# Kernel tuning notes

Measured on AMD Instinct MI355X. Metric: run time of the kernel, lower is better.

The kernel has to match this reference:

```python
import jax, jax.numpy as jnp
import numpy as np

N = 131072       # total nodes (B graphs x P nodes)
P = 4096         # nodes per graph
B = 32           # graphs in batch
E = 2097152      # edges (avg degree 16)
IN_DIM = 64
HID = 128
OUT = 16
EPS = 1e-5
SLOPE = 0.01


def _degrees(idx):
    # structural degree, clamped to min 1 (as DGL GraphConv does)
    d = jax.ops.segment_sum(jnp.ones((E,), jnp.float32), idx, num_segments=N)
    return jnp.maximum(d, 1.0)


def _graph_conv(x, W, src, dst, ew):
    # DGL GraphConv, norm='both', bias=False, with scalar edge weights:
    # h = D_out^{-1/2} x ; m_v = sum_{(u->v)} w_e h_u ; out = (D_in^{-1/2} m) W
    h = x * jax.lax.rsqrt(_degrees(src))[:, None]
    m = jax.ops.segment_sum(ew[:, None] * h[src], dst, num_segments=N)  # [N, F]
    return (m * jax.lax.rsqrt(_degrees(dst))[:, None]) @ W


def _graph_norm(x, gamma, beta, alpha):
    # GraphNorm (Cai et al. / PyG, batch=None): stats over all nodes per feature
    mu = jnp.mean(x, axis=0)
    c = x - alpha * mu
    var = jnp.mean(c * c, axis=0)
    return c * jax.lax.rsqrt(var + EPS) * gamma + beta


def _mean_nodes(h, gid):
    # per-graph mean readout; every graph has exactly P nodes
    return jax.ops.segment_sum(h, gid, num_segments=B) / P


def setup_inputs() -> dict:
    key = jax.random.key(0)
    ks = jax.random.split(key, 8)
    src = jax.random.randint(ks[0], (E,), 0, N, dtype=jnp.int32)
    # keep edges within each 4096-node graph block (batched DGL graph)
    dst = (src // P) * P + jax.random.randint(ks[1], (E,), 0, P, dtype=jnp.int32)
    features = jax.random.normal(ks[2], (N, IN_DIM), jnp.float32)
    edge_weights = jax.random.uniform(ks[3], (E,), jnp.float32)
    # kaiming/xavier-scale init approximations
    W1 = jax.random.normal(ks[4], (IN_DIM, HID), jnp.float32) * np.sqrt(2.0 / IN_DIM)
    W2 = jax.random.normal(ks[5], (HID, HID), jnp.float32) * np.sqrt(2.0 / HID)
    Wc = jax.random.normal(ks[6], (OUT, 2 * HID), jnp.float32) * np.sqrt(1.0 / (2 * HID))
    ones = jnp.ones((HID,), jnp.float32)
    zeros = jnp.zeros((HID,), jnp.float32)
    return {
        'features': features, 'edge_weights': edge_weights, 'src': src, 'dst': dst,
        'W1': W1, 'W2': W2, 'Wc': Wc,
        'gamma1': ones, 'beta1': zeros, 'alpha1': ones,
        'gamma2': ones, 'beta2': zeros, 'alpha2': ones,
    }


def reference(features, edge_weights, src, dst, W1, W2, Wc,
              gamma1, beta1, alpha1, gamma2, beta2, alpha2):
    gid = jnp.arange(N, dtype=jnp.int32) // P  # node -> graph id
    h1 = _graph_conv(features, W1, src, dst, edge_weights)
    h1 = jax.nn.leaky_relu(_graph_norm(h1, gamma1, beta1, alpha1), SLOPE)
    r1 = _mean_nodes(h1, gid)                  # [B, HID]
    h2 = _graph_conv(h1, W2, src, dst, edge_weights)
    h2 = jax.nn.leaky_relu(_graph_norm(h2, gamma2, beta2, alpha2), SLOPE)
    r2 = _mean_nodes(h2, gid)                  # [B, HID]
    readouts = jnp.concatenate([r1, r2], axis=1)  # [B, 2*HID]
    return readouts @ Wc.T                     # [B, OUT]
```

## Files before the change

kernel.cpp:

```cpp
#include <hip/hip_runtime.h>
#include <hip/hip_fp16.h>

constexpr int NN   = 131072;
constexpr int PP   = 4096;
constexpr int BG   = 32;
constexpr int EE   = 2097152;
constexpr int IND  = 64;
constexpr int HH   = 128;
constexpr int CAP  = 81920;
constexpr float EPSV   = 1e-5f;
constexpr float SLOPEV = 0.01f;

typedef _Float16 h16x8 __attribute__((ext_vector_type(8)));
typedef float f32x4  __attribute__((ext_vector_type(4)));
typedef unsigned u32x4 __attribute__((ext_vector_type(4)));

__device__ __forceinline__ __half2 bits2h(unsigned u) { __half2 h; *(unsigned*)&h = u; return h; }
__device__ __forceinline__ unsigned h2bits(__half2 h) { return *(unsigned*)&h; }

template <int K>
__device__ __forceinline__ void packw_body(const float* __restrict__ W,
                                           unsigned short* __restrict__ pw, int t) {
    if (t >= K * 16) return;
    int lane = t & 63, nt = (t >> 6) & 7, kt = t >> 9;
    int kbase = kt * 32 + ((lane >> 4) & 3) * 8;
    int col   = nt * 16 + (lane & 15);
    for (int j = 0; j < 8; j++)
        pw[t * 8 + j] = __half_as_ushort(__float2half_rn(W[(kbase + j) * HH + col]));
}

__global__ __launch_bounds__(256) void k_prep(const float* __restrict__ features,
                                              unsigned* __restrict__ f16x,
                                              const float* __restrict__ W1,
                                              unsigned short* __restrict__ pw1,
                                              const float* __restrict__ W2,
                                              unsigned short* __restrict__ pw2,
                                              int* __restrict__ gcur,
                                              float* __restrict__ racc,
                                              unsigned* __restrict__ csr2) {
    int b = blockIdx.x, t = threadIdx.x;
    if (b < 8192) {
        int i = b * 256 + t;
        float4 v = ((const float4*)features)[i];
        __half2 lo = __floats2half2_rn(v.x, v.y);
        __half2 hi = __floats2half2_rn(v.z, v.w);
        ((uint2*)f16x)[i] = make_uint2(h2bits(lo), h2bits(hi));
        return;
    }
    if (b == 8192) {
        if (t < BG) gcur[t * 16] = t * CAP;
        for (int i = t; i < 2 * BG * HH; i += 256) racc[i] = 0.f;
        return;
    }
    if (b < 8197) { packw_body<64>(W1, pw1, (b - 8193) * 256 + t); return; }
    if (b < 8205) { packw_body<128>(W2, pw2, (b - 8197) * 256 + t); return; }
    ((uint4*)csr2)[(b - 8205) * 256 + t] = make_uint4(0, 0, 0, 0);
}

__global__ __launch_bounds__(256) void k_part(const int* __restrict__ src,
                                              const int* __restrict__ dst,
                                              const float* __restrict__ ew,
                                              int* __restrict__ gcur,
                                              uint2* __restrict__ recs) {
    __shared__ int cnt[32];
    __shared__ int start[32];
    __shared__ int gbase[32];
    __shared__ uint2 stage[4096];
    int t = threadIdx.x;
    int ebase = blockIdx.x * 4096;
    if (t < 32) cnt[t] = 0;
    __syncthreads();
    int es[16]; int ed[16]; float ev[16];
#pragma unroll
    for (int k = 0; k < 16; k++) {
        int e = ebase + k * 256 + t;
        es[k] = src[e]; ed[k] = dst[e]; ev[k] = ew[e];
        atomicAdd(&cnt[es[k] >> 12], 1);
    }
    __syncthreads();
    if (t == 0) {
        int run = 0;
        for (int g = 0; g < 32; g++) { start[g] = run; run += cnt[g]; }
    }
    __syncthreads();
    if (t < 32) {
        gbase[t] = atomicAdd(&gcur[t * 16], cnt[t]);
        cnt[t] = start[t];
    }
    __syncthreads();
#pragma unroll
    for (int k = 0; k < 16; k++) {
        int g = es[k] >> 12;
        int pos = atomicAdd(&cnt[g], 1);
        stage[pos] = make_uint2((unsigned)(es[k] & 4095) | ((unsigned)(ed[k] & 4095) << 12) |
                                ((unsigned)g << 24), __float_as_uint(ev[k]));
    }
    __syncthreads();
    for (int i = t; i < 4096; i += 256) {
        uint2 r = stage[i];
        int g = r.x >> 24;
        recs[gbase[g] + (i - start[g])] = r;
    }
}

__global__ __launch_bounds__(1024) void k_hist(const uint2* __restrict__ recs,
                                               const int* __restrict__ gcur,
                                               int* __restrict__ shist,
                                               int* __restrict__ dhist) {
    __shared__ int hs[4096];
    __shared__ int hd[4096];
    int t = threadIdx.x;
    int g = blockIdx.x >> 3, c = blockIdx.x & 7;
    int n = gcur[g * 16] - g * CAP;
    int lo = (n * c) >> 3, hi = (n * (c + 1)) >> 3;
    ((int4*)hs)[t] = make_int4(0, 0, 0, 0);
    ((int4*)hd)[t] = make_int4(0, 0, 0, 0);
    __syncthreads();
    const uint2* base = recs + (size_t)g * CAP;
    for (int i = lo + t; i < hi; i += 1024) {
        unsigned x = base[i].x;
        atomicAdd(&hs[x & 4095], 1);
        atomicAdd(&hd[(x >> 12) & 4095], 1);
    }
    __syncthreads();
    ((int4*)(shist + (size_t)blockIdx.x * 4096))[t] = ((int4*)hs)[t];
    ((int4*)(dhist + (size_t)blockIdx.x * 4096))[t] = ((int4*)hd)[t];
}

__global__ __launch_bounds__(1024) void k_offs(int* __restrict__ shist,
                                               int* __restrict__ dhist,
                                               float* __restrict__ rs_s,
                                               float* __restrict__ rsd,
                                               int* __restrict__ degd,
                                               int* __restrict__ offs) {
    __shared__ int partial[1024];
    int t = threadIdx.x, g = blockIdx.x;
    int sdeg[4] = {0, 0, 0, 0}, ddeg[4] = {0, 0, 0, 0};
#pragma unroll
    for (int c = 0; c < 8; c++) {
        int4 sv = ((const int4*)(shist + (size_t)(g * 8 + c) * 4096))[t];
        int4 dv = ((const int4*)(dhist + (size_t)(g * 8 + c) * 4096))[t];
        sdeg[0] += sv.x; sdeg[1] += sv.y; sdeg[2] += sv.z; sdeg[3] += sv.w;
        ddeg[0] += dv.x; ddeg[1] += dv.y; ddeg[2] += dv.z; ddeg[3] += dv.w;
    }
    int pdeg[4];
#pragma unroll
    for (int j = 0; j < 4; j++) {
        int idx = t * 4 + j;
        int vs = sdeg[j]; if (vs < 1) vs = 1;
        rs_s[g * PP + idx] = rsqrtf((float)vs);
        int vd = ddeg[j]; if (vd < 1) vd = 1;
        rsd[g * PP + idx]  = rsqrtf((float)vd);
        pdeg[j] = (ddeg[j] + 3) & ~3;
        degd[g * PP + idx] = pdeg[j];
    }
    partial[t] = pdeg[0] + pdeg[1] + pdeg[2] + pdeg[3];
    __syncthreads();
    for (int off = 1; off < 1024; off <<= 1) {
        int v = partial[t];
        int add = (t >= off) ? partial[t - off] : 0;
        __syncthreads();
        partial[t] = v + add;
        __syncthreads();
    }
    int run = (t == 0) ? 0 : partial[t - 1];
#pragma unroll
    for (int j = 0; j < 4; j++) {
        int idx = t * 4 + j;
        offs[g * PP + idx] = g * CAP + run;
        int nb = run;
        for (int c = 0; c < 8; c++) {
            size_t hidx = (size_t)(g * 8 + c) * 4096 + idx;
            int v = dhist[hidx];
            dhist[hidx] = nb;
            nb += v;
        }
        run += pdeg[j];
    }
}

__global__ __launch_bounds__(1024) void k_place(const uint2* __restrict__ recs,
                                                const int* __restrict__ gcur,
                                                const int* __restrict__ dhist,
                                                const float* __restrict__ rs_s,
                                                unsigned* __restrict__ csr2) {
    __shared__ int cur[4096];
    __shared__ float rss[4096];
    int t = threadIdx.x;
    int g = blockIdx.x >> 3, c = blockIdx.x & 7;
    int n = gcur[g * 16] - g * CAP;
    int lo = (n * c) >> 3, hi = (n * (c + 1)) >> 3;
    ((int4*)cur)[t] = ((const int4*)(dhist + (size_t)blockIdx.x * 4096))[t];
    ((float4*)rss)[t] = ((const float4*)(rs_s + (size_t)g * PP))[t];
    __syncthreads();
    const uint2* base = recs + (size_t)g * CAP;
    unsigned* cbase = csr2 + (size_t)g * CAP;
    for (int i = lo + t; i < hi; i += 1024) {
        uint2 r = base[i];
        int sl = r.x & 4095, dl = (r.x >> 12) & 4095;
        int pos = atomicAdd(&cur[dl], 1);
        float wf = __uint_as_float(r.y) * rss[sl];
        cbase[pos] = (unsigned)sl | ((unsigned)__half_as_ushort(__float2half(wf)) << 16);
    }
}

__device__ __forceinline__ void edge_acc(unsigned rec, uint2 q, __half2& P01, __half2& P23) {
    unsigned wb = __builtin_amdgcn_perm(rec, rec, 0x03020302u);
    __half2 w2 = bits2h(wb);
    P01 = __hfma2(w2, bits2h(q.x), P01);
    P23 = __hfma2(w2, bits2h(q.y), P23);
}

template <int ROWW>
__device__ __forceinline__ void gath(const uint2* __restrict__ gb, unsigned loff, u32x4 r,
                                     uint2& d0, uint2& d1, uint2& d2, uint2& d3) {
    d0 = gb[(r[0] & 4095u) * ROWW + loff];
    d1 = gb[(r[1] & 4095u) * ROWW + loff];
    d2 = gb[(r[2] & 4095u) * ROWW + loff];
    d3 = gb[(r[3] & 4095u) * ROWW + loff];
}

__device__ __forceinline__ void macc(u32x4 r, uint2 q0, uint2 q1, uint2 q2, uint2 q3,
                                     __half2& P01, __half2& P23) {
    edge_acc(r[0], q0, P01, P23); edge_acc(r[1], q1, P01, P23);
    edge_acc(r[2], q2, P01, P23); edge_acc(r[3], q3, P01, P23);
}

template <int ROWW>
__device__ __forceinline__ void agg_dual(const uint2* __restrict__ gb, unsigned loff,
                                         const u32x4* __restrict__ cs4,
                                         int oa, int ca, int ob, int cb,
                                         __half2& A01, __half2& A23,
                                         __half2& B01, __half2& B23) {
    A01 = __float2half2_rn(0.f); A23 = A01; B01 = A01; B23 = A01;
    unsigned a4 = ((unsigned)oa) >> 2, b4 = ((unsigned)ob) >> 2;
    int c0 = ca < cb ? ca : cb;
    int cm = ca < cb ? cb : ca;
    int nq = c0 >> 2;
    if (nq > 0) {
        u32x4 ra0 = __builtin_nontemporal_load(cs4 + a4);
        u32x4 rb0 = __builtin_nontemporal_load(cs4 + b4);
        u32x4 ra1 = __builtin_nontemporal_load(cs4 + a4 + 1);
        u32x4 rb1 = __builtin_nontemporal_load(cs4 + b4 + 1);
        uint2 A0, A1, A2, A3, B0, B1, B2, B3;
        uint2 C0, C1, C2, C3, D0, D1, D2, D3;
        gath<ROWW>(gb, loff, ra0, A0, A1, A2, A3);
        gath<ROWW>(gb, loff, rb0, B0, B1, B2, B3);
        int k = 0;
        for (; k + 2 <= nq; k += 2) {
            gath<ROWW>(gb, loff, ra1, C0, C1, C2, C3);
            gath<ROWW>(gb, loff, rb1, D0, D1, D2, D3);
            u32x4 ra2 = __builtin_nontemporal_load(cs4 + a4 + k + 2);
            u32x4 rb2 = __builtin_nontemporal_load(cs4 + b4 + k + 2);
            macc(ra0, A0, A1, A2, A3, A01, A23);
            macc(rb0, B0, B1, B2, B3, B01, B23);
            gath<ROWW>(gb, loff, ra2, A0, A1, A2, A3);
            gath<ROWW>(gb, loff, rb2, B0, B1, B2, B3);
            u32x4 ra3 = __builtin_nontemporal_load(cs4 + a4 + k + 3);
            u32x4 rb3 = __builtin_nontemporal_load(cs4 + b4 + k + 3);
            macc(ra1, C0, C1, C2, C3, A01, A23);
            macc(rb1, D0, D1, D2, D3, B01, B23);
            ra0 = ra2; rb0 = rb2; ra1 = ra3; rb1 = rb3;
        }
        if (k < nq) {
            macc(ra0, A0, A1, A2, A3, A01, A23);
            macc(rb0, B0, B1, B2, B3, B01, B23);
        }
    }
    if (cm > c0) {
        bool an = ca > cb;
        unsigned t4 = an ? a4 : b4;
        int kq1 = cm >> 2;
        __half2 E01 = __float2half2_rn(0.f), E23 = E01;
        int nq0 = c0 >> 2;
        u32x4 rr = __builtin_nontemporal_load(cs4 + t4 + nq0);
        for (int k = nq0; k < kq1; k++) {
            uint2 q0, q1, q2, q3;
            gath<ROWW>(gb, loff, rr, q0, q1, q2, q3);
            u32x4 nr = __builtin_nontemporal_load(cs4 + t4 + k + 1);
            macc(rr, q0, q1, q2, q3, E01, E23);
            rr = nr;
        }
        if (an) { A01 = __hadd2(A01, E01); A23 = __hadd2(A23, E23); }
        else    { B01 = __hadd2(B01, E01); B23 = __hadd2(B23, E23); }
    }
}

__global__ __launch_bounds__(256) void k_aggemm1(const unsigned* __restrict__ fx,
                                                 const unsigned* __restrict__ csr2,
                                                 const int* __restrict__ offs,
                                                 const int* __restrict__ degd,
                                                 const float* __restrict__ rsd,
                                                 const unsigned short* __restrict__ PW,
                                                 unsigned short* __restrict__ C,
                                                 float* __restrict__ part) {
    constexpr int WP = 36;
    __shared__ __align__(16) unsigned lds[64 * WP];
    __shared__ float s1[HH], s2[HH];
    int t = threadIdx.x;
    if (t < HH) { s1[t] = 0.f; s2[t] = 0.f; }
    int bid = blockIdx.x;
    int xcd = bid & 7, idx = bid >> 3;
    int g = xcd * 4 + (idx >> 6);
    int node0 = g * PP + (idx & 63) * 64;
    int lane = t & 63, wv = t >> 6;
    int q = lane >> 4, ql = lane & 15;
    const uint2* gb = (const uint2*)fx + (size_t)((unsigned)(g * PP)) * 16;
    const u32x4* cs4 = (const u32x4*)csr2;
#pragma unroll
    for (int p = 0; p < 2; p++) {
        int lrA = wv * 16 + p * 8 + q * 2;
        int va = node0 + lrA;
        int2 oo = *(const int2*)(offs + va);
        int2 dd = *(const int2*)(degd + va);
        __half2 A01, A23, B01, B23;
        agg_dual<16>(gb, (unsigned)ql, cs4, oo.x, dd.x, oo.y, dd.y, A01, A23, B01, B23);
        float2 rr2 = *(const float2*)(rsd + va);
        __half2 ha = __float2half2_rn(rr2.x), hb = __float2half2_rn(rr2.y);
        __half2 a0 = __hmul2(A01, ha), a1 = __hmul2(A23, ha);
        __half2 b0 = __hmul2(B01, hb), b1 = __hmul2(B23, hb);
        *(uint2*)&lds[lrA * WP + ql * 2]       = make_uint2(h2bits(a0), h2bits(a1));
        *(uint2*)&lds[(lrA + 1) * WP + ql * 2] = make_uint2(h2bits(b0), h2bits(b1));
    }
    __syncthreads();
    int m = lane & 15, quad = lane >> 4;
    h16x8 a[2];
#pragma unroll
    for (int kt = 0; kt < 2; kt++)
        a[kt] = *(const h16x8*)&lds[(wv * 16 + m) * WP + kt * 16 + quad * 4];
#pragma unroll
    for (int nt = 0; nt < 8; nt++) {
        f32x4 acc = {0.f, 0.f, 0.f, 0.f};
#pragma unroll
        for (int kt = 0; kt < 2; kt++) {
            h16x8 b = *(const h16x8*)(PW + ((size_t)(kt * 8 + nt) * 64 + lane) * 8);
            acc = __builtin_amdgcn_mfma_f32_16x16x32_f16(a[kt], b, acc, 0, 0, 0);
        }
        int col = nt * 16 + m;
        int r0 = node0 + wv * 16 + quad * 4;
        float ps = 0.f, pq = 0.f;
#pragma unroll
        for (int r = 0; r < 4; r++) {
            __builtin_nontemporal_store(
                (unsigned short)__half_as_ushort(__float2half_rn(acc[r])),
                &C[(size_t)(r0 + r) * HH + col]);
            ps += acc[r]; pq += acc[r] * acc[r];
        }
        atomicAdd(&s1[col], ps);
        atomicAdd(&s2[col], pq);
    }
    __syncthreads();
    if (t < HH) {
        __builtin_nontemporal_store(s1[t], &part[bid * 256 + t]);
        __builtin_nontemporal_store(s2[t], &part[bid * 256 + HH + t]);
    }
}

__global__ __launch_bounds__(256) void k_aggemm2(const unsigned* __restrict__ hsrc,
                                                 const unsigned* __restrict__ csr2,
                                                 const int* __restrict__ offs,
                                                 const int* __restrict__ degd,
                                                 const float* __restrict__ rsd,
                                                 const unsigned short* __restrict__ PW,
                                                 unsigned short* __restrict__ C,
                                                 float* __restrict__ part) {
    constexpr int WP = 68;
    __shared__ __align__(16) unsigned lds[64 * WP];
    __shared__ float s1[HH], s2[HH];
    int t = threadIdx.x;
    if (t < HH) { s1[t] = 0.f; s2[t] = 0.f; }
    int bid = blockIdx.x;
    int xcd = bid & 7, idx = bid >> 3;
    int g = xcd * 4 + (idx >> 6);
    int node0 = g * PP + (idx & 63) * 64;
    int lane = t & 63, wv = t >> 6;
    int half = lane >> 5, sl = lane & 31;
    const uint2* gb = (const uint2*)hsrc + (size_t)((unsigned)(g * PP)) * 32;
    const u32x4* cs4 = (const u32x4*)csr2;
#pragma unroll
    for (int p = 0; p < 4; p++) {
        int lrA = wv * 16 + p * 4 + half * 2;
        int va = node0 + lrA;
        int2 oo = *(const int2*)(offs + va);
        int2 dd = *(const int2*)(degd + va);
        __half2 A01, A23, B01, B23;
        agg_dual<32>(gb, (unsigned)sl, cs4, oo.x, dd.x, oo.y, dd.y, A01, A23, B01, B23);
        float2 rr2 = *(const float2*)(rsd + va);
        __half2 ha = __float2half2_rn(rr2.x), hb = __float2half2_rn(rr2.y);
        __half2 a0 = __hmul2(A01, ha), a1 = __hmul2(A23, ha);
        __half2 b0 = __hmul2(B01, hb), b1 = __hmul2(B23, hb);
        *(uint2*)&lds[lrA * WP + sl * 2]       = make_uint2(h2bits(a0), h2bits(a1));
        *(uint2*)&lds[(lrA + 1) * WP + sl * 2] = make_uint2(h2bits(b0), h2bits(b1));
    }
    __syncthreads();
    int m = lane & 15, quad = lane >> 4;
    h16x8 a[4];
#pragma unroll
    for (int kt = 0; kt < 4; kt++)
        a[kt] = *(const h16x8*)&lds[(wv * 16 + m) * WP + kt * 16 + quad * 4];
#pragma unroll
    for (int nt = 0; nt < 8; nt++) {
        f32x4 acc = {0.f, 0.f, 0.f, 0.f};
#pragma unroll
        for (int kt = 0; kt < 4; kt++) {
            h16x8 b = *(const h16x8*)(PW + ((size_t)(kt * 8 + nt) * 64 + lane) * 8);
            acc = __builtin_amdgcn_mfma_f32_16x16x32_f16(a[kt], b, acc, 0, 0, 0);
        }
        int col = nt * 16 + m;
        int r0 = node0 + wv * 16 + quad * 4;
        float ps = 0.f, pq = 0.f;
#pragma unroll
        for (int r = 0; r < 4; r++) {
            __builtin_nontemporal_store(
                (unsigned short)__half_as_ushort(__float2half_rn(acc[r])),
                &C[(size_t)(r0 + r) * HH + col]);
            ps += acc[r]; pq += acc[r] * acc[r];
        }
        atomicAdd(&s1[col], ps);
        atomicAdd(&s2[col], pq);
    }
    __syncthreads();
    if (t < HH) {
        __builtin_nontemporal_store(s1[t], &part[bid * 256 + t]);
        __builtin_nontemporal_store(s2[t], &part[bid * 256 + HH + t]);
    }
}

__global__ __launch_bounds__(256) void k_red(const float* __restrict__ part,
                                             float* __restrict__ pb) {
    int t = threadIdx.x, b = blockIdx.x;
    float s = 0.f;
    for (int r = 0; r < 32; r++) s += part[(size_t)(b * 32 + r) * 256 + t];
    pb[b * 256 + t] = s;
}

__global__ void k_coef(const float* __restrict__ pb, const float* __restrict__ gamma,
                       const float* __restrict__ beta, const float* __restrict__ alpha,
                       float* __restrict__ ab) {
    int t = threadIdx.x;
    float s = 0.f;
    for (int b = 0; b < 64; b++) s += pb[b * 256 + t];
    __shared__ float sh[256];
    sh[t] = s;
    __syncthreads();
    if (t < 128) {
        float mu = sh[t] * (1.f / NN);
        float e2 = sh[128 + t] * (1.f / NN);
        float al = alpha[t];
        float var = e2 - (2.f * al - al * al) * mu * mu;
        float a = rsqrtf(var + EPSV) * gamma[t];
        ab[t] = a;
        ab[HH + t] = beta[t] - al * mu * a;
    }
}

template <bool WRITE>
__global__ __launch_bounds__(256) void k_normro(const unsigned* __restrict__ h,
                                                const float* __restrict__ ab,
                                                float* __restrict__ racc,
                                                unsigned* __restrict__ f16o) {
    int fp = threadIdx.x & 63;
    int q  = threadIdx.x >> 6;
    int node0 = blockIdx.x * 64;
    int g = node0 / PP;
    float a0 = ab[2 * fp], a1 = ab[2 * fp + 1];
    float b0 = ab[HH + 2 * fp], b1 = ab[HH + 2 * fp + 1];
    float s0 = 0.f, s1 = 0.f;
    for (int i = q; i < 64; i += 4) {
        size_t idx = (size_t)(node0 + i) * 64 + fp;
        unsigned v = __builtin_nontemporal_load(&h[idx]);
        __half2 hv = bits2h(v);
        float x0 = fmaf(a0, __low2float(hv),  b0); x0 = x0 > 0.f ? x0 : SLOPEV * x0;
        float x1 = fmaf(a1, __high2float(hv), b1); x1 = x1 > 0.f ? x1 : SLOPEV * x1;
        if (WRITE) {
            __half2 o = __floats2half2_rn(x0, x1);
            __builtin_nontemporal_store(h2bits(o), &f16o[idx]);
        }
        s0 += x0; s1 += x1;
    }
    __shared__ float sh[512];
    sh[threadIdx.x] = s0;
    sh[256 + threadIdx.x] = s1;
    __syncthreads();
    if (q == 0) {
        float t0 = s0 + sh[64 + fp] + sh[128 + fp] + sh[192 + fp];
        float t1 = s1 + sh[256 + 64 + fp] + sh[256 + 128 + fp] + sh[256 + 192 + fp];
        atomicAdd(&racc[g * HH + 2 * fp],     t0);
        atomicAdd(&racc[g * HH + 2 * fp + 1], t1);
    }
}

__global__ void k_final(const float* __restrict__ racc1, const float* __restrict__ racc2,
                        const float* __restrict__ Wc, float* __restrict__ out) {
    int t = threadIdx.x;
    int b = t >> 4, o = t & 15;
    float acc = 0.f;
    for (int f = 0; f < HH; f++) acc += racc1[b * HH + f] * Wc[o * (2 * HH) + f];
    for (int f = 0; f < HH; f++) acc += racc2[b * HH + f] * Wc[o * (2 * HH) + HH + f];
    out[t] = acc * (1.f / PP);
}

extern "C" void kernel_launch(void* const* d_in, const int* in_sizes, int n_in,
                              void* d_out, int out_size, void* d_ws, size_t ws_size,
                              hipStream_t stream) {
    const float* features = (const float*)d_in[0];
    const float* ew       = (const float*)d_in[1];
    const int*   src      = (const int*)d_in[2];
    const int*   dst      = (const int*)d_in[3];
    const float* W1       = (const float*)d_in[4];
    const float* W2       = (const float*)d_in[5];
    const float* Wc       = (const float*)d_in[6];
    const float* gamma1   = (const float*)d_in[7];
    const float* beta1    = (const float*)d_in[8];
    const float* alpha1   = (const float*)d_in[9];
    const float* gamma2   = (const float*)d_in[10];
    const float* beta2    = (const float*)d_in[11];
    const float* alpha2   = (const float*)d_in[12];
    float* out = (float*)d_out;

    char* w = (char*)d_ws;
    int*    gcur   = (int*)(w + 0);
    float*  racc1  = (float*)(w + (16u << 10));
    float*  racc2  = (float*)(w + (32u << 10));
    float*  ab1    = (float*)(w + (48u << 10));
    float*  ab2    = (float*)(w + (52u << 10));
    unsigned short* pw1 = (unsigned short*)(w + (64u << 10));
    unsigned short* pw2 = (unsigned short*)(w + (80u << 10));
    float*  pb     = (float*)(w + (128u << 10));
    float*  rs_s   = (float*)(w + (1024u << 10));
    float*  rsd    = (float*)(w + (1536u << 10));
    int*    degd   = (int*)(w + (2048u << 10));
    int*    offs   = (int*)(w + (2560u << 10));
    float*  part   = (float*)(w + (3u << 20));
    int*    shist  = (int*)(w + (5u << 20));
    int*    dhist  = (int*)(w + (9u << 20));
    unsigned* csr2 = (unsigned*)(w + (13u << 20));
    unsigned* mbuf = (unsigned*)(w + (23u << 20));
    unsigned* hbuf = (unsigned*)(w + (55u << 20));
    uint2*    recs = (uint2*)(w + (87u << 20));
    unsigned* f16x = (unsigned*)(w + (107u << 20));

    k_prep<<<10765, 256, 0, stream>>>(features, f16x, W1, pw1, W2, pw2, gcur, racc1, csr2);

    k_part<<<EE / 4096, 256, 0, stream>>>(src, dst, ew, gcur, recs);
    k_hist<<<BG * 8, 1024, 0, stream>>>(recs, gcur, shist, dhist);
    k_offs<<<BG, 1024, 0, stream>>>(shist, dhist, rs_s, rsd, degd, offs);
    k_place<<<BG * 8, 1024, 0, stream>>>(recs, gcur, dhist, rs_s, csr2);

    k_aggemm1<<<NN / 64, 256, 0, stream>>>(f16x, csr2, offs, degd, rsd,
                                           pw1, (unsigned short*)hbuf, part);
    k_red<<<64, 256, 0, stream>>>(part, pb);
    k_coef<<<1, 256, 0, stream>>>(pb, gamma1, beta1, alpha1, ab1);
    k_normro<true><<<NN / 64, 256, 0, stream>>>(hbuf, ab1, racc1, mbuf);

    k_aggemm2<<<NN / 64, 256, 0, stream>>>(mbuf, csr2, offs, degd, rsd,
                                           pw2, (unsigned short*)hbuf, part);
    k_red<<<64, 256, 0, stream>>>(part, pb);
    k_coef<<<1, 256, 0, stream>>>(pb, gamma2, beta2, alpha2, ab2);
    k_normro<false><<<NN / 64, 256, 0, stream>>>(hbuf, ab2, racc2, nullptr);

    k_final<<<1, 512, 0, stream>>>(racc1, racc2, Wc, out);
}
```

Measured before the change: 419.4 us.

## Store gathered node features in fp8 and switch GEMMs and outputs to bf16

Input features and the layer-1 activations that feed layer 2 are now stored as packed fp8 (4 bytes per 4 features instead of 8). Each edge gather therefore reads half as many bytes, and the edge accumulation moves from fp16 half2 FMAs to fp32 after unpacking the fp8 values. The MFMA GEMMs now use bf16 operands, the pre-norm outputs are stored as bf16, and nontemporal hints on those stores and loads are dropped. fp8 quantisation of activations lowers accuracy and may break the tolerance, and the extra unpack instructions add ALU work per edge.

```diff
diff --git a/kernel.cpp b/kernel.cpp
--- a/kernel.cpp
+++ b/kernel.cpp
@@ -11,12 +11,23 @@
 constexpr float EPSV   = 1e-5f;
 constexpr float SLOPEV = 0.01f;
 
-typedef _Float16 h16x8 __attribute__((ext_vector_type(8)));
+typedef short bf16x8 __attribute__((ext_vector_type(8)));
 typedef float f32x4  __attribute__((ext_vector_type(4)));
+typedef float f32x2  __attribute__((ext_vector_type(2)));
 typedef unsigned u32x4 __attribute__((ext_vector_type(4)));
 
-__device__ __forceinline__ __half2 bits2h(unsigned u) { __half2 h; *(unsigned*)&h = u; return h; }
-__device__ __forceinline__ unsigned h2bits(__half2 h) { return *(unsigned*)&h; }
+__device__ __forceinline__ unsigned f2bf(float f) {
+    unsigned u = __float_as_uint(f);
+    return (u + 0x7FFFu + ((u >> 16) & 1u)) >> 16;
+}
+__device__ __forceinline__ unsigned pack2bf(float lo, float hi) {
+    return f2bf(lo) | (f2bf(hi) << 16);
+}
+__device__ __forceinline__ float bflo(unsigned p) { return __uint_as_float(p << 16); }
+__device__ __forceinline__ float bfhi(unsigned p) { return __uint_as_float(p & 0xFFFF0000u); }
+__device__ __forceinline__ float w16(unsigned r) {
+    return __half2float(__ushort_as_half((unsigned short)(r >> 16)));
+}
 
 template <int K>
 __device__ __forceinline__ void packw_body(const float* __restrict__ W,
@@ -26,11 +37,11 @@
     int kbase = kt * 32 + ((lane >> 4) & 3) * 8;
     int col   = nt * 16 + (lane & 15);
     for (int j = 0; j < 8; j++)
-        pw[t * 8 + j] = __half_as_ushort(__float2half_rn(W[(kbase + j) * HH + col]));
+        pw[t * 8 + j] = (unsigned short)f2bf(W[(kbase + j) * HH + col]);
 }
 
 __global__ __launch_bounds__(256) void k_prep(const float* __restrict__ features,
-                                              unsigned* __restrict__ f16x,
+                                              unsigned* __restrict__ f8x,
                                               const float* __restrict__ W1,
                                               unsigned short* __restrict__ pw1,
                                               const float* __restrict__ W2,
@@ -42,9 +53,9 @@
     if (b < 8192) {
         int i = b * 256 + t;
         float4 v = ((const float4*)features)[i];
-        __half2 lo = __floats2half2_rn(v.x, v.y);
-        __half2 hi = __floats2half2_rn(v.z, v.w);
-        ((uint2*)f16x)[i] = make_uint2(h2bits(lo), h2bits(hi));
+        int w0 = __builtin_amdgcn_cvt_pk_fp8_f32(v.x, v.y, 0, false);
+        int w1 = __builtin_amdgcn_cvt_pk_fp8_f32(v.z, v.w, w0, true);
+        f8x[i] = (unsigned)w1;
         return;
     }
     if (b == 8192) {
@@ -204,35 +215,36 @@
     }
 }
 
-__device__ __forceinline__ void edge_acc(unsigned rec, uint2 q, __half2& P01, __half2& P23) {
-    unsigned wb = __builtin_amdgcn_perm(rec, rec, 0x03020302u);
-    __half2 w2 = bits2h(wb);
-    P01 = __hfma2(w2, bits2h(q.x), P01);
-    P23 = __hfma2(w2, bits2h(q.y), P23);
+__device__ __forceinline__ void eacc8(unsigned rec, unsigned q, f32x2& P01, f32x2& P23) {
+    f32x2 lo = __builtin_amdgcn_cvt_pk_f32_fp8((int)q, false);
+    f32x2 hi = __builtin_amdgcn_cvt_pk_f32_fp8((int)q, true);
+    float w = w16(rec);
+    P01 += lo * w;
+    P23 += hi * w;
 }
 
 template <int ROWW>
-__device__ __forceinline__ void gath(const uint2* __restrict__ gb, unsigned loff, u32x4 r,
-                                     uint2& d0, uint2& d1, uint2& d2, uint2& d3) {
-    d0 = gb[(r[0] & 4095u) * ROWW + loff];
-    d1 = gb[(r[1] & 4095u) * ROWW + loff];
-    d2 = gb[(r[2] & 4095u) * ROWW + loff];
-    d3 = gb[(r[3] & 4095u) * ROWW + loff];
-}
-
-__device__ __forceinline__ void macc(u32x4 r, uint2 q0, uint2 q1, uint2 q2, uint2 q3,
-                                     __half2& P01, __half2& P23) {
-    edge_acc(r[0], q0, P01, P23); edge_acc(r[1], q1, P01, P23);
-    edge_acc(r[2], q2, P01, P23); edge_acc(r[3], q3, P01, P23);
+__device__ __forceinline__ void gath8(const unsigned* __restrict__ hp, u32x4 r,
+                                      unsigned& d0, unsigned& d1, unsigned& d2, unsigned& d3) {
+    d0 = hp[(r[0] & 4095u) * ROWW];
+    d1 = hp[(r[1] & 4095u) * ROWW];
+    d2 = hp[(r[2] & 4095u) * ROWW];
+    d3 = hp[(r[3] & 4095u) * ROWW];
+}
+
+__device__ __forceinline__ void macc8(u32x4 r, unsigned q0, unsigned q1, unsigned q2, unsigned q3,
+                                      f32x2& P01, f32x2& P23) {
+    eacc8(r[0], q0, P01, P23); eacc8(r[1], q1, P01, P23);
+    eacc8(r[2], q2, P01, P23); eacc8(r[3], q3, P01, P23);
 }
 
 template <int ROWW>
-__device__ __forceinline__ void agg_dual(const uint2* __restrict__ gb, unsigned loff,
-                                         const u32x4* __restrict__ cs4,
-                                         int oa, int ca, int ob, int cb,
-                                         __half2& A01, __half2& A23,
-                                         __half2& B01, __half2& B23) {
-    A01 = __float2half2_rn(0.f); A23 = A01; B01 = A01; B23 = A01;
+__device__ __forceinline__ void agg_dual8(const unsigned* __restrict__ hp,
+                                          const u32x4* __restrict__ cs4,
+                                          int oa, int ca, int ob, int cb,
+                                          f32x2& A01, f32x2& A23, f32x2& B01, f32x2& B23) {
+    f32x2 z = {0.f, 0.f};
+    A01 = z; A23 = z; B01 = z; B23 = z;
     unsigned a4 = ((unsigned)oa) >> 2, b4 = ((unsigned)ob) >> 2;
     int c0 = ca < cb ? ca : cb;
     int cm = ca < cb ? cb : ca;
@@ -242,60 +254,59 @@
         u32x4 rb0 = __builtin_nontemporal_load(cs4 + b4);
         u32x4 ra1 = __builtin_nontemporal_load(cs4 + a4 + 1);
         u32x4 rb1 = __builtin_nontemporal_load(cs4 + b4 + 1);
-        uint2 A0, A1, A2, A3, B0, B1, B2, B3;
-        uint2 C0, C1, C2, C3, D0, D1, D2, D3;
-        gath<ROWW>(gb, loff, ra0, A0, A1, A2, A3);
-        gath<ROWW>(gb, loff, rb0, B0, B1, B2, B3);
+        unsigned A0, A1, A2, A3, B0, B1, B2, B3;
+        unsigned C0, C1, C2, C3, D0, D1, D2, D3;
+        gath8<ROWW>(hp, ra0, A0, A1, A2, A3);
+        gath8<ROWW>(hp, rb0, B0, B1, B2, B3);
         int k = 0;
         for (; k + 2 <= nq; k += 2) {
-            gath<ROWW>(gb, loff, ra1, C0, C1, C2, C3);
-            gath<ROWW>(gb, loff, rb1, D0, D1, D2, D3);
+            gath8<ROWW>(hp, ra1, C0, C1, C2, C3);
+            gath8<ROWW>(hp, rb1, D0, D1, D2, D3);
             u32x4 ra2 = __builtin_nontemporal_load(cs4 + a4 + k + 2);
             u32x4 rb2 = __builtin_nontemporal_load(cs4 + b4 + k + 2);
-            macc(ra0, A0, A1, A2, A3, A01, A23);
-            macc(rb0, B0, B1, B2, B3, B01, B23);
-            gath<ROWW>(gb, loff, ra2, A0, A1, A2, A3);
-            gath<ROWW>(gb, loff, rb2, B0, B1, B2, B3);
+            macc8(ra0, A0, A1, A2, A3, A01, A23);
+            macc8(rb0, B0, B1, B2, B3, B01, B23);
+            gath8<ROWW>(hp, ra2, A0, A1, A2, A3);
+            gath8<ROWW>(hp, rb2, B0, B1, B2, B3);
             u32x4 ra3 = __builtin_nontemporal_load(cs4 + a4 + k + 3);
             u32x4 rb3 = __builtin_nontemporal_load(cs4 + b4 + k + 3);
-            macc(ra1, C0, C1, C2, C3, A01, A23);
-            macc(rb1, D0, D1, D2, D3, B01, B23);
+            macc8(ra1, C0, C1, C2, C3, A01, A23);
+            macc8(rb1, D0, D1, D2, D3, B01, B23);
             ra0 = ra2; rb0 = rb2; ra1 = ra3; rb1 = rb3;
         }
         if (k < nq) {
-            macc(ra0, A0, A1, A2, A3, A01, A23);
-            macc(rb0, B0, B1, B2, B3, B01, B23);
+            macc8(ra0, A0, A1, A2, A3, A01, A23);
+            macc8(rb0, B0, B1, B2, B3, B01, B23);
         }
     }
     if (cm > c0) {
         bool an = ca > cb;
         unsigned t4 = an ? a4 : b4;
-        int kq1 = cm >> 2;
-        __half2 E01 = __float2half2_rn(0.f), E23 = E01;
-        int nq0 = c0 >> 2;
+        int kq1 = cm >> 2, nq0 = c0 >> 2;
+        f32x2 E01 = z, E23 = z;
         u32x4 rr = __builtin_nontemporal_load(cs4 + t4 + nq0);
         for (int k = nq0; k < kq1; k++) {
-            uint2 q0, q1, q2, q3;
-            gath<ROWW>(gb, loff, rr, q0, q1, q2, q3);
+            unsigned q0, q1, q2, q3;
+            gath8<ROWW>(hp, rr, q0, q1, q2, q3);
             u32x4 nr = __builtin_nontemporal_load(cs4 + t4 + k + 1);
-            macc(rr, q0, q1, q2, q3, E01, E23);
+            macc8(rr, q0, q1, q2, q3, E01, E23);
             rr = nr;
         }
-        if (an) { A01 = __hadd2(A01, E01); A23 = __hadd2(A23, E23); }
-        else    { B01 = __hadd2(B01, E01); B23 = __hadd2(B23, E23); }
-    }
-}
-
-__global__ __launch_bounds__(256) void k_aggemm1(const unsigned* __restrict__ fx,
+        if (an) { A01 += E01; A23 += E23; }
+        else    { B01 += E01; B23 += E23; }
+    }
+}
+
+__global__ __launch_bounds__(256) void k_aggemm1(const unsigned* __restrict__ f8x,
                                                  const unsigned* __restrict__ csr2,
                                                  const int* __restrict__ offs,
                                                  const int* __restrict__ degd,
                                                  const float* __restrict__ rsd,
-                                                 const unsigned short* __restrict__ PW,
+                                                 const short* __restrict__ PW,
                                                  unsigned short* __restrict__ C,
                                                  float* __restrict__ part) {
     constexpr int WP = 36;
-    __shared__ __align__(16) unsigned lds[64 * WP];
+    __shared__ unsigned lds[64 * WP];
     __shared__ float s1[HH], s2[HH];
     int t = threadIdx.x;
     if (t < HH) { s1[t] = 0.f; s2[t] = 0.f; }
@@ -305,7 +316,7 @@
     int node0 = g * PP + (idx & 63) * 64;
     int lane = t & 63, wv = t >> 6;
     int q = lane >> 4, ql = lane & 15;
-    const uint2* gb = (const uint2*)fx + (size_t)((unsigned)(g * PP)) * 16;
+    const unsigned* hp8 = f8x + (size_t)((unsigned)(g * PP)) * 16 + ql;
     const u32x4* cs4 = (const u32x4*)csr2;
 #pragma unroll
     for (int p = 0; p < 2; p++) {
@@ -313,37 +324,36 @@
         int va = node0 + lrA;
         int2 oo = *(const int2*)(offs + va);
         int2 dd = *(const int2*)(degd + va);
-        __half2 A01, A23, B01, B23;
-        agg_dual<16>(gb, (unsigned)ql, cs4, oo.x, dd.x, oo.y, dd.y, A01, A23, B01, B23);
+        f32x2 A01, A23, B01, B23;
+        agg_dual8<16>(hp8, cs4, oo.x, dd.x, oo.y, dd.y, A01, A23, B01, B23);
         float2 rr2 = *(const float2*)(rsd + va);
-        __half2 ha = __float2half2_rn(rr2.x), hb = __float2half2_rn(rr2.y);
-        __half2 a0 = __hmul2(A01, ha), a1 = __hmul2(A23, ha);
-        __half2 b0 = __hmul2(B01, hb), b1 = __hmul2(B23, hb);
-        *(uint2*)&lds[lrA * WP + ql * 2]       = make_uint2(h2bits(a0), h2bits(a1));
-        *(uint2*)&lds[(lrA + 1) * WP + ql * 2] = make_uint2(h2bits(b0), h2bits(b1));
+        *(uint2*)&lds[lrA * WP + ql * 2] =
+            make_uint2(pack2bf(A01.x * rr2.x, A01.y * rr2.x),
+                       pack2bf(A23.x * rr2.x, A23.y * rr2.x));
+        *(uint2*)&lds[(lrA + 1) * WP + ql * 2] =
+            make_uint2(pack2bf(B01.x * rr2.y, B01.y * rr2.y),
+                       pack2bf(B23.x * rr2.y, B23.y * rr2.y));
     }
     __syncthreads();
     int m = lane & 15, quad = lane >> 4;
-    h16x8 a[2];
+    bf16x8 a[2];
 #pragma unroll
     for (int kt = 0; kt < 2; kt++)
-        a[kt] = *(const h16x8*)&lds[(wv * 16 + m) * WP + kt * 16 + quad * 4];
+        a[kt] = *(const bf16x8*)&lds[(wv * 16 + m) * WP + kt * 16 + quad * 4];
 #pragma unroll
     for (int nt = 0; nt < 8; nt++) {
         f32x4 acc = {0.f, 0.f, 0.f, 0.f};
 #pragma unroll
         for (int kt = 0; kt < 2; kt++) {
-            h16x8 b = *(const h16x8*)(PW + ((size_t)(kt * 8 + nt) * 64 + lane) * 8);
-            acc = __builtin_amdgcn_mfma_f32_16x16x32_f16(a[kt], b, acc, 0, 0, 0);
+            bf16x8 b = *(const bf16x8*)(PW + ((size_t)(kt * 8 + nt) * 64 + lane) * 8);
+            acc = __builtin_amdgcn_mfma_f32_16x16x32_bf16(a[kt], b, acc, 0, 0, 0);
         }
         int col = nt * 16 + m;
         int r0 = node0 + wv * 16 + quad * 4;
         float ps = 0.f, pq = 0.f;
 #pragma unroll
         for (int r = 0; r < 4; r++) {
-            __builtin_nontemporal_store(
-                (unsigned short)__half_as_ushort(__float2half_rn(acc[r])),
-                &C[(size_t)(r0 + r) * HH + col]);
+            C[(size_t)(r0 + r) * HH + col] = (unsigned short)f2bf(acc[r]);
             ps += acc[r]; pq += acc[r] * acc[r];
         }
         atomicAdd(&s1[col], ps);
@@ -351,21 +361,21 @@
     }
     __syncthreads();
     if (t < HH) {
-        __builtin_nontemporal_store(s1[t], &part[bid * 256 + t]);
-        __builtin_nontemporal_store(s2[t], &part[bid * 256 + HH + t]);
-    }
-}
-
-__global__ __launch_bounds__(256) void k_aggemm2(const unsigned* __restrict__ hsrc,
+        part[bid * 256 + t]      = s1[t];
+        part[bid * 256 + HH + t] = s2[t];
+    }
+}
+
+__global__ __launch_bounds__(256) void k_aggemm2(const unsigned* __restrict__ f8,
                                                  const unsigned* __restrict__ csr2,
                                                  const int* __restrict__ offs,
                                                  const int* __restrict__ degd,
                                                  const float* __restrict__ rsd,
-                                                 const unsigned short* __restrict__ PW,
+                                                 const short* __restrict__ PW,
                                                  unsigned short* __restrict__ C,
                                                  float* __restrict__ part) {
     constexpr int WP = 68;
-    __shared__ __align__(16) unsigned lds[64 * WP];
+    __shared__ unsigned lds[64 * WP];
     __shared__ float s1[HH], s2[HH];
     int t = threadIdx.x;
     if (t < HH) { s1[t] = 0.f; s2[t] = 0.f; }
@@ -375,7 +385,7 @@
     int node0 = g * PP + (idx & 63) * 64;
     int lane = t & 63, wv = t >> 6;
     int half = lane >> 5, sl = lane & 31;
-    const uint2* gb = (const uint2*)hsrc + (size_t)((unsigned)(g * PP)) * 32;
+    const unsigned* hp8 = f8 + (size_t)((unsigned)(g * PP)) * 32 + sl;
     const u32x4* cs4 = (const u32x4*)csr2;
 #pragma unroll
     for (int p = 0; p < 4; p++) {
@@ -383,37 +393,36 @@
         int va = node0 + lrA;
         int2 oo = *(const int2*)(offs + va);
         int2 dd = *(const int2*)(degd + va);
-        __half2 A01, A23, B01, B23;
-        agg_dual<32>(gb, (unsigned)sl, cs4, oo.x, dd.x, oo.y, dd.y, A01, A23, B01, B23);
+        f32x2 A01, A23, B01, B23;
+        agg_dual8<32>(hp8, cs4, oo.x, dd.x, oo.y, dd.y, A01, A23, B01, B23);
         float2 rr2 = *(const float2*)(rsd + va);
-        __half2 ha = __float2half2_rn(rr2.x), hb = __float2half2_rn(rr2.y);
-        __half2 a0 = __hmul2(A01, ha), a1 = __hmul2(A23, ha);
-        __half2 b0 = __hmul2(B01, hb), b1 = __hmul2(B23, hb);
-        *(uint2*)&lds[lrA * WP + sl * 2]       = make_uint2(h2bits(a0), h2bits(a1));
-        *(uint2*)&lds[(lrA + 1) * WP + sl * 2] = make_uint2(h2bits(b0), h2bits(b1));
+        *(uint2*)&lds[lrA * WP + sl * 2] =
+            make_uint2(pack2bf(A01.x * rr2.x, A01.y * rr2.x),
+                       pack2bf(A23.x * rr2.x, A23.y * rr2.x));
+        *(uint2*)&lds[(lrA + 1) * WP + sl * 2] =
+            make_uint2(pack2bf(B01.x * rr2.y, B01.y * rr2.y),
+                       pack2bf(B23.x * rr2.y, B23.y * rr2.y));
     }
     __syncthreads();
     int m = lane & 15, quad = lane >> 4;
-    h16x8 a[4];
+    bf16x8 a[4];
 #pragma unroll
     for (int kt = 0; kt < 4; kt++)
-        a[kt] = *(const h16x8*)&lds[(wv * 16 + m) * WP + kt * 16 + quad * 4];
+        a[kt] = *(const bf16x8*)&lds[(wv * 16 + m) * WP + kt * 16 + quad * 4];
 #pragma unroll
     for (int nt = 0; nt < 8; nt++) {
         f32x4 acc = {0.f, 0.f, 0.f, 0.f};
 #pragma unroll
         for (int kt = 0; kt < 4; kt++) {
-            h16x8 b = *(const h16x8*)(PW + ((size_t)(kt * 8 + nt) * 64 + lane) * 8);
-            acc = __builtin_amdgcn_mfma_f32_16x16x32_f16(a[kt], b, acc, 0, 0, 0);
+            bf16x8 b = *(const bf16x8*)(PW + ((size_t)(kt * 8 + nt) * 64 + lane) * 8);
+            acc = __builtin_amdgcn_mfma_f32_16x16x32_bf16(a[kt], b, acc, 0, 0, 0);
         }
         int col = nt * 16 + m;
         int r0 = node0 + wv * 16 + quad * 4;
         float ps = 0.f, pq = 0.f;
 #pragma unroll
         for (int r = 0; r < 4; r++) {
-            __builtin_nontemporal_store(
-                (unsigned short)__half_as_ushort(__float2half_rn(acc[r])),
-                &C[(size_t)(r0 + r) * HH + col]);
+            C[(size_t)(r0 + r) * HH + col] = (unsigned short)f2bf(acc[r]);
             ps += acc[r]; pq += acc[r] * acc[r];
         }
         atomicAdd(&s1[col], ps);
@@ -421,8 +430,8 @@
     }
     __syncthreads();
     if (t < HH) {
-        __builtin_nontemporal_store(s1[t], &part[bid * 256 + t]);
-        __builtin_nontemporal_store(s2[t], &part[bid * 256 + HH + t]);
+        part[bid * 256 + t]      = s1[t];
+        part[bid * 256 + HH + t] = s2[t];
     }
 }
 
@@ -458,7 +467,7 @@
 __global__ __launch_bounds__(256) void k_normro(const unsigned* __restrict__ h,
                                                 const float* __restrict__ ab,
                                                 float* __restrict__ racc,
-                                                unsigned* __restrict__ f16o) {
+                                                unsigned short* __restrict__ f8) {
     int fp = threadIdx.x & 63;
     int q  = threadIdx.x >> 6;
     int node0 = blockIdx.x * 64;
@@ -468,14 +477,10 @@
     float s0 = 0.f, s1 = 0.f;
     for (int i = q; i < 64; i += 4) {
         size_t idx = (size_t)(node0 + i) * 64 + fp;
-        unsigned v = __builtin_nontemporal_load(&h[idx]);
-        __half2 hv = bits2h(v);
-        float x0 = fmaf(a0, __low2float(hv),  b0); x0 = x0 > 0.f ? x0 : SLOPEV * x0;
-        float x1 = fmaf(a1, __high2float(hv), b1); x1 = x1 > 0.f ? x1 : SLOPEV * x1;
-        if (WRITE) {
-            __half2 o = __floats2half2_rn(x0, x1);
-            __builtin_nontemporal_store(h2bits(o), &f16o[idx]);
-        }
+        unsigned v = h[idx];
+        float x0 = fmaf(a0, bflo(v), b0); x0 = x0 > 0.f ? x0 : SLOPEV * x0;
+        float x1 = fmaf(a1, bfhi(v), b1); x1 = x1 > 0.f ? x1 : SLOPEV * x1;
+        if (WRITE) f8[idx] = (unsigned short)__builtin_amdgcn_cvt_pk_fp8_f32(x0, x1, 0, false);
         s0 += x0; s1 += x1;
     }
     __shared__ float sh[512];
@@ -538,26 +543,27 @@
     unsigned* mbuf = (unsigned*)(w + (23u << 20));
     unsigned* hbuf = (unsigned*)(w + (55u << 20));
     uint2*    recs = (uint2*)(w + (87u << 20));
-    unsigned* f16x = (unsigned*)(w + (107u << 20));
-
-    k_prep<<<10765, 256, 0, stream>>>(features, f16x, W1, pw1, W2, pw2, gcur, racc1, csr2);
+    unsigned* f8x  = (unsigned*)(w + (107u << 20));
+    unsigned* f8buf= (unsigned*)(w + (123u << 20));
+
+    k_prep<<<10765, 256, 0, stream>>>(features, f8x, W1, pw1, W2, pw2, gcur, racc1, csr2);
 
     k_part<<<EE / 4096, 256, 0, stream>>>(src, dst, ew, gcur, recs);
     k_hist<<<BG * 8, 1024, 0, stream>>>(recs, gcur, shist, dhist);
     k_offs<<<BG, 1024, 0, stream>>>(shist, dhist, rs_s, rsd, degd, offs);
     k_place<<<BG * 8, 1024, 0, stream>>>(recs, gcur, dhist, rs_s, csr2);
 
-    k_aggemm1<<<NN / 64, 256, 0, stream>>>(f16x, csr2, offs, degd, rsd,
-                                           pw1, (unsigned short*)hbuf, part);
+    k_aggemm1<<<NN / 64, 256, 0, stream>>>(f8x, csr2, offs, degd, rsd,
+                                           (const short*)pw1, (unsigned short*)hbuf, part);
     k_red<<<64, 256, 0, stream>>>(part, pb);
     k_coef<<<1, 256, 0, stream>>>(pb, gamma1, beta1, alpha1, ab1);
-    k_normro<true><<<NN / 64, 256, 0, stream>>>(hbuf, ab1, racc1, mbuf);
-
-    k_aggemm2<<<NN / 64, 256, 0, stream>>>(mbuf, csr2, offs, degd, rsd,
-                                           pw2, (unsigned short*)hbuf, part);
+    k_normro<true><<<NN / 64, 256, 0, stream>>>(hbuf, ab1, racc1, (unsigned short*)f8buf);
+
+    k_aggemm2<<<NN / 64, 256, 0, stream>>>(f8buf, csr2, offs, degd, rsd,
+                                           (const short*)pw2, (unsigned short*)mbuf, part);
     k_red<<<64, 256, 0, stream>>>(part, pb);
     k_coef<<<1, 256, 0, stream>>>(pb, gamma2, beta2, alpha2, ab2);
-    k_normro<false><<<NN / 64, 256, 0, stream>>>(hbuf, ab2, racc2, nullptr);
+    k_normro<false><<<NN / 64, 256, 0, stream>>>(mbuf, ab2, racc2, nullptr);
 
     k_final<<<1, 512, 0, stream>>>(racc1, racc2, Wc, out);
 }
```

Result: faster. 370.7 us (-11.6%).
